# Performance work log

Hardware: AMD Instinct MI355X
Metric: run time of the kernel (lower is better)

Reference implementation:

```python
import jax, jax.numpy as jnp
import numpy as np

HID = 512
HEADS = 8
DH = HID // HEADS


def setup_inputs() -> dict:
    key = jax.random.key(0)
    ks = jax.random.split(key, 20)
    B, L = 4, 256
    s = 1.0 / np.sqrt(HID)
    sh = 1.0 / np.sqrt(DH)
    inp = {
        'query': jax.random.normal(ks[0], (B, L, HID), jnp.float32),
        'key':   jax.random.normal(ks[1], (B, L, HID), jnp.float32),
        'value': jax.random.normal(ks[2], (B, L, HID), jnp.float32),
        'Wq': jax.random.uniform(ks[3], (HID, HID), jnp.float32, -s, s),
        'bq': jax.random.uniform(ks[4], (HID,), jnp.float32, -s, s),
        'Wk': jax.random.uniform(ks[5], (HID, HID), jnp.float32, -s, s),
        'bk': jax.random.uniform(ks[6], (HID,), jnp.float32, -s, s),
        'Wv': jax.random.uniform(ks[7], (HID, HID), jnp.float32, -s, s),
        'bv': jax.random.uniform(ks[8], (HID,), jnp.float32, -s, s),
        'W1': jax.random.uniform(ks[9], (DH, DH), jnp.float32, -sh, sh),
        'b1': jax.random.uniform(ks[10], (DH,), jnp.float32, -sh, sh),
        'W2': jax.random.uniform(ks[11], (DH, DH), jnp.float32, -sh, sh),
        'b2': jax.random.uniform(ks[12], (DH,), jnp.float32, -sh, sh),
        'va_w': jax.random.uniform(ks[13], (1, DH), jnp.float32, -sh, sh),
        'va_b': jax.random.uniform(ks[14], (1,), jnp.float32, -sh, sh),
        'Wo': jax.random.uniform(ks[15], (HID, HID), jnp.float32, -s, s),
        'bo': jax.random.uniform(ks[16], (HID,), jnp.float32, -s, s),
    }
    return inp


def reference(query, key, value, Wq, bq, Wk, bk, Wv, bv, W1, b1, W2, b2, va_w, va_b, Wo, bo):
    B, Lq, _ = query.shape
    Lk = key.shape[1]
    # projections + split heads -> [B, H, L, Dh]
    Q = (query @ Wq.T + bq).reshape(B, Lq, HEADS, DH).transpose(0, 2, 1, 3)
    K = (key   @ Wk.T + bk).reshape(B, Lk, HEADS, DH).transpose(0, 2, 1, 3)
    V = (value @ Wv.T + bv).reshape(B, Lk, HEADS, DH).transpose(0, 2, 1, 3)
    Qt = Q @ W1.T + b1  # [B,H,Lq,Dh]
    Kt = K @ W2.T + b2  # [B,H,Lk,Dh]
    # additive (Bahdanau) scores: va . tanh(q_i + k_j) + b over head_dim
    pair = jnp.tanh(Qt[:, :, :, None, :] + Kt[:, :, None, :, :])  # [B,H,Lq,Lk,Dh]
    energy = jnp.einsum('bhqkd,d->bhqk', pair, va_w[0]) + va_b[0]
    attention = jax.nn.softmax(energy, axis=-1)
    x = jnp.einsum('bhqk,bhkd->bhqd', attention, V)
    x = x.transpose(0, 2, 1, 3).reshape(B, Lq, HID)
    out = x @ Wo.T + bo
    return out, attention
```

## Files before the change

### kernel.cpp

```cpp
#include <hip/hip_runtime.h>

#define HIDN 512
#define NHEAD 8
#define DHEAD 64
#define NB 4
#define NL 256
#define NROW 1024

#define SCALE2 2.8853900817779268f
#define LOG2E  1.4426950408889634f
#define NEG2LOG2E -2.8853900817779268f

#define WS_WQB 0
#define WS_WKB (WS_WQB + 131072)
#define WS_BQF (WS_WKB + 131072)
#define WS_BKF (WS_BQF + 512)
#define WS_QBF (WS_BKF + 512)
#define WS_KBF (WS_QBF + 262144)
#define WS_VBF (WS_KBF + 262144)
#define WS_WVB (WS_VBF + 262144)
#define WS_WOB (WS_WVB + 131072)
#define WS_EQ  (WS_WOB + 131072)
#define WS_EK  (WS_EQ + 524288)
#define WS_VF  (WS_EK + 524288)

typedef __attribute__((ext_vector_type(4))) float f32x4;
typedef __attribute__((ext_vector_type(8))) short bf16x8;

__device__ __forceinline__ short f2bf(float x) {
  unsigned u = __float_as_uint(x);
  u += 0x7fffu + ((u >> 16) & 1u);
  return (short)(u >> 16);
}

__global__ __launch_bounds__(256) void prep(
    const float* __restrict__ Wq, const float* __restrict__ bq,
    const float* __restrict__ Wk, const float* __restrict__ bk,
    const float* __restrict__ W1, const float* __restrict__ b1,
    const float* __restrict__ W2, const float* __restrict__ b2,
    const float* __restrict__ q, const float* __restrict__ k, const float* __restrict__ v,
    const float* __restrict__ Wv, const float* __restrict__ Wo,
    float* __restrict__ ws)
{
  const int z = blockIdx.z;
  if (z >= 2) {
    const int zz = z - 2;
    const float* src; short* dst; int n;
    if (zz == 0)      { src = q;  dst = (short*)(ws + WS_QBF); n = 524288; }
    else if (zz == 1) { src = k;  dst = (short*)(ws + WS_KBF); n = 524288; }
    else if (zz == 2) { src = v;  dst = (short*)(ws + WS_VBF); n = 524288; }
    else if (zz == 3) { src = Wv; dst = (short*)(ws + WS_WVB); n = 262144; }
    else              { src = Wo; dst = (short*)(ws + WS_WOB); n = 262144; }
    const int i = (blockIdx.x * 256 + threadIdx.x) * 8;
    if (i >= n) return;
    const float4 a = *reinterpret_cast<const float4*>(src + i);
    const float4 b = *reinterpret_cast<const float4*>(src + i + 4);
    bf16x8 o;
    o[0] = f2bf(a.x); o[1] = f2bf(a.y); o[2] = f2bf(a.z); o[3] = f2bf(a.w);
    o[4] = f2bf(b.x); o[5] = f2bf(b.y); o[6] = f2bf(b.z); o[7] = f2bf(b.w);
    *reinterpret_cast<bf16x8*>(dst + i) = o;
    return;
  }

  if (blockIdx.x >= 128) return;
  const int c0 = (blockIdx.x & 3) * 128;
  const int y  = blockIdx.x >> 2;
  const int h  = y >> 2;
  const int ig = y & 3;
  const int which = z;
  const float* Wsrc = which ? Wk : Wq;
  const float* bsrc = which ? bk : bq;
  const float* Wt   = which ? W2 : W1;
  const float* bt   = which ? b2 : b1;
  short* Wout = reinterpret_cast<short*>(ws + (which ? WS_WKB : WS_WQB));
  float* bout = ws + (which ? WS_BKF : WS_BQF);

  __shared__ float Wtl[16][68];
  for (int t = threadIdx.x; t < 16*64; t += 256)
    Wtl[t >> 6][t & 63] = Wt[(ig*16 + (t >> 6))*64 + (t & 63)];
  __syncthreads();

  const int c  = c0 + (threadIdx.x & 127);
  const int i0 = (threadIdx.x >> 7) * 8;
  float acc[8];
#pragma unroll
  for (int ii = 0; ii < 8; ++ii) acc[ii] = 0.f;

  for (int j0 = 0; j0 < 64; j0 += 4) {
    const float s0 = Wsrc[(h*64 + j0 + 0)*HIDN + c];
    const float s1 = Wsrc[(h*64 + j0 + 1)*HIDN + c];
    const float s2 = Wsrc[(h*64 + j0 + 2)*HIDN + c];
    const float s3 = Wsrc[(h*64 + j0 + 3)*HIDN + c];
#pragma unroll
    for (int ii = 0; ii < 8; ++ii) {
      const float4 wv4 = *reinterpret_cast<const float4*>(&Wtl[i0+ii][j0]);
      float a = acc[ii];
      a = fmaf(wv4.x, s0, a);
      a = fmaf(wv4.y, s1, a);
      a = fmaf(wv4.z, s2, a);
      a = fmaf(wv4.w, s3, a);
      acc[ii] = a;
    }
  }
#pragma unroll
  for (int ii = 0; ii < 8; ++ii)
    Wout[(h*64 + ig*16 + i0 + ii)*HIDN + c] = f2bf(acc[ii] * SCALE2);

  if (blockIdx.x == 0 && threadIdx.x < 16) {
    const int il = threadIdx.x;
    float a = bt[ig*16 + il];
    for (int j = 0; j < 64; ++j)
      a = fmaf(Wtl[il][j], bsrc[h*64 + j], a);
    bout[h*64 + ig*16 + il] = a * SCALE2;
  }
}

__global__ __launch_bounds__(256) void mfma_proj(float* __restrict__ ws, const float* __restrict__ bv)
{
  const int z = blockIdx.z;
  const short* A; const short* W; const float* bias;
  if (z == 0)      { A = (const short*)(ws + WS_QBF); W = (const short*)(ws + WS_WQB); bias = ws + WS_BQF; }
  else if (z == 1) { A = (const short*)(ws + WS_KBF); W = (const short*)(ws + WS_WKB); bias = ws + WS_BKF; }
  else             { A = (const short*)(ws + WS_VBF); W = (const short*)(ws + WS_WVB); bias = bv; }

  const int wid  = threadIdx.x >> 6;
  const int lane = threadIdx.x & 63;
  const int mt = blockIdx.y * 4 + wid;
  const int nb = blockIdx.x * 32;
  const short* aptr = A + (mt*16 + (lane & 15))*HIDN + (lane >> 4)*8;
  const short* wptr = W + (nb + (lane & 15))*HIDN + (lane >> 4)*8;

  f32x4 acc[2] = {{0,0,0,0},{0,0,0,0}};
#pragma unroll 4
  for (int k0 = 0; k0 < HIDN; k0 += 32) {
    const bf16x8 af = *reinterpret_cast<const bf16x8*>(aptr + k0);
    const short* wp = wptr + k0;
#pragma unroll
    for (int t = 0; t < 2; ++t)
      acc[t] = __builtin_amdgcn_mfma_f32_16x16x32_bf16(
          af, *reinterpret_cast<const bf16x8*>(wp + t*16*HIDN), acc[t], 0, 0, 0);
  }

  const int rbase = mt*16 + (lane >> 4)*4;
  if (z < 2) {
    float* dst = ws + (z == 0 ? WS_EQ : WS_EK);
#pragma unroll
    for (int t = 0; t < 2; ++t) {
      const int c = nb + t*16 + (lane & 15);
      const float bc = bias[c];
      const int hh = c >> 6, d = c & 63;
#pragma unroll
      for (int r = 0; r < 4; ++r) {
        const int R = rbase + r;
        dst[(((R >> 8)*NHEAD + hh)*NL + (R & 255))*DHEAD + d] =
            __builtin_amdgcn_exp2f(acc[t][r] + bc);
      }
    }
  } else {
    short* vf = reinterpret_cast<short*>(ws + WS_VF);
#pragma unroll
    for (int t = 0; t < 2; ++t) {
      const int c = nb + t*16 + (lane & 15);
      const float bc = bias[c];
      const int hh = c >> 6, d = c & 63;
#pragma unroll
      for (int r = 0; r < 4; ++r) {
        const int R = rbase + r;
        const int l = R & 255;
        const int bh = (R >> 8)*NHEAD + hh;
        const int tile = ((l >> 5) << 2) + (d >> 4);
        const int lanep = (((l >> 3) & 3) << 4) + (d & 15);
        vf[((bh*32 + tile)*64 + lanep)*8 + (l & 7)] = f2bf(acc[t][r] + bc);
      }
    }
  }
}

__global__ __launch_bounds__(256) void mfma_out(
    float* __restrict__ ws, const float* __restrict__ bo, float* __restrict__ out)
{
  const short* A = (const short*)(ws + WS_QBF);
  const short* W = (const short*)(ws + WS_WOB);
  const int wid  = threadIdx.x >> 6;
  const int lane = threadIdx.x & 63;
  const int mt = blockIdx.y * 4 + wid;
  const int nb = blockIdx.x * 32;
  const short* aptr = A + (mt*16 + (lane & 15))*HIDN + (lane >> 4)*8;
  const short* wptr = W + (nb + (lane & 15))*HIDN + (lane >> 4)*8;

  f32x4 acc[2] = {{0,0,0,0},{0,0,0,0}};
#pragma unroll 4
  for (int k0 = 0; k0 < HIDN; k0 += 32) {
    const bf16x8 af = *reinterpret_cast<const bf16x8*>(aptr + k0);
    const short* wp = wptr + k0;
#pragma unroll
    for (int t = 0; t < 2; ++t)
      acc[t] = __builtin_amdgcn_mfma_f32_16x16x32_bf16(
          af, *reinterpret_cast<const bf16x8*>(wp + t*16*HIDN), acc[t], 0, 0, 0);
  }

  const int rbase = mt*16 + (lane >> 4)*4;
#pragma unroll
  for (int t = 0; t < 2; ++t) {
    const int c = nb + t*16 + (lane & 15);
    const float bc = bo[c];
#pragma unroll
    for (int r = 0; r < 4; ++r)
      out[(rbase + r)*HIDN + c] = acc[t][r] + bc;
  }
}

__global__ __launch_bounds__(1024, 8) void attn_kernel(
    const float* __restrict__ eqB, const float* __restrict__ ekB,
    const short* __restrict__ vfB, const float* __restrict__ va_w,
    float* __restrict__ attn_out, short* __restrict__ xb)
{
  const int qt = blockIdx.x;
  const int bh = blockIdx.y;
  const int tid = threadIdx.x;

  __shared__ __align__(16) short aLb[8][64][8];
  __shared__ __align__(16) float reds[4][4][4];

  const float* EKB = ekB + bh*NL*DHEAD;
  const short* VF  = vfB + bh*32*64*8;

  const int g  = tid >> 8;
  const int lk = tid & 255;
  const int wv = lk >> 6;
  const int l  = lk & 63;
  const float* EkRow = EKB + lk*DHEAD;
  const int g_u = __builtin_amdgcn_readfirstlane(g);
  const float* EqG = eqB + (bh*NL + qt*16 + g_u*4)*DHEAD;

  float acc[4];
#pragma unroll
  for (int qi = 0; qi < 4; ++qi) acc[qi] = 0.f;

#pragma unroll 1
  for (int d0 = 0; d0 < 64; d0 += 8) {
    const f32x4 ea = *reinterpret_cast<const f32x4*>(EkRow + d0);
    const f32x4 eb = *reinterpret_cast<const f32x4*>(EkRow + d0 + 4);
    const f32x4 vaA = *reinterpret_cast<const f32x4*>(va_w + d0);
    const f32x4 vaB = *reinterpret_cast<const f32x4*>(va_w + d0 + 4);
#pragma unroll
    for (int qi = 0; qi < 4; ++qi) {
      const f32x4 qa = *reinterpret_cast<const f32x4*>(EqG + qi*DHEAD + d0);
      const f32x4 qb = *reinterpret_cast<const f32x4*>(EqG + qi*DHEAD + d0 + 4);
      const float t0 = fmaf(qa.x, ea.x, 1.0f);
      const float t1 = fmaf(qa.y, ea.y, 1.0f);
      const float t2 = fmaf(qa.z, ea.z, 1.0f);
      const float t3 = fmaf(qa.w, ea.w, 1.0f);
      const float t4 = fmaf(qb.x, eb.x, 1.0f);
      const float t5 = fmaf(qb.y, eb.y, 1.0f);
      const float t6 = fmaf(qb.z, eb.z, 1.0f);
      const float t7 = fmaf(qb.w, eb.w, 1.0f);
      float a = acc[qi];
      a = fmaf(fmaf(vaA.x, t1, vaA.y * t0), __builtin_amdgcn_rcpf(t0 * t1), a);
      a = fmaf(fmaf(vaA.z, t3, vaA.w * t2), __builtin_amdgcn_rcpf(t2 * t3), a);
      a = fmaf(fmaf(vaB.x, t5, vaB.y * t4), __builtin_amdgcn_rcpf(t4 * t5), a);
      a = fmaf(fmaf(vaB.z, t7, vaB.w * t6), __builtin_amdgcn_rcpf(t6 * t7), a);
      acc[qi] = a;
    }
  }

  float p[4];
#pragma unroll
  for (int qi = 0; qi < 4; ++qi)
    p[qi] = __builtin_amdgcn_exp2f(acc[qi] * NEG2LOG2E);

#pragma unroll
  for (int qi = 0; qi < 4; ++qi) {
    float s = p[qi];
#pragma unroll
    for (int off = 1; off < 64; off <<= 1)
      s += __shfl_xor(s, off);
    if (l == 0) reds[g][wv][qi] = s;
  }
  {
    const int kb2 = lk >> 5;
    const int lbase = ((lk >> 3) & 3) * 16;
    const int jb = lk & 7;
#pragma unroll
    for (int qi = 0; qi < 4; ++qi)
      aLb[kb2][lbase + g*4 + qi][jb] = f2bf(p[qi]);
  }
  __syncthreads();

  {
    f32x4 s4 = {0.f,0.f,0.f,0.f};
#pragma unroll
    for (int w2 = 0; w2 < 4; ++w2)
      s4 += *reinterpret_cast<const f32x4*>(&reds[g][w2][0]);
    float inv[4];
    inv[0] = __builtin_amdgcn_rcpf(s4.x); inv[1] = __builtin_amdgcn_rcpf(s4.y);
    inv[2] = __builtin_amdgcn_rcpf(s4.z); inv[3] = __builtin_amdgcn_rcpf(s4.w);
#pragma unroll
    for (int qi = 0; qi < 4; ++qi)
      attn_out[(bh*NL + qt*16 + g*4 + qi)*NL + lk] = p[qi] * inv[qi];

    const int wid = tid >> 6;
    if (wid < 4) {
      f32x4 pacc = {0.f,0.f,0.f,0.f};
#pragma unroll
      for (int kb2 = 0; kb2 < 8; ++kb2) {
        const bf16x8 af  = *reinterpret_cast<const bf16x8*>(&aLb[kb2][l][0]);
        const bf16x8 bff = *reinterpret_cast<const bf16x8*>(&VF[((kb2*4 + wid)*64 + l)*8]);
        pacc = __builtin_amdgcn_mfma_f32_16x16x32_bf16(af, bff, pacc, 0, 0, 0);
      }
      const int b_ = bh >> 3, hh = bh & 7;
      const int colv = hh*DHEAD + wid*16 + (l & 15);
#pragma unroll
      for (int r = 0; r < 4; ++r) {
        const int row = (l >> 4)*4 + r;
        const float stot = reds[row>>2][0][row&3] + reds[row>>2][1][row&3]
                         + reds[row>>2][2][row&3] + reds[row>>2][3][row&3];
        xb[(b_*NL + qt*16 + row)*HIDN + colv] = f2bf(pacc[r] * __builtin_amdgcn_rcpf(stot));
      }
    }
  }
}

extern "C" void kernel_launch(void* const* d_in, const int* in_sizes, int n_in,
                              void* d_out, int out_size, void* d_ws, size_t ws_size,
                              hipStream_t stream) {
  const float* query = (const float*)d_in[0];
  const float* key   = (const float*)d_in[1];
  const float* value = (const float*)d_in[2];
  const float* Wq = (const float*)d_in[3];
  const float* bq = (const float*)d_in[4];
  const float* Wk = (const float*)d_in[5];
  const float* bk = (const float*)d_in[6];
  const float* Wv = (const float*)d_in[7];
  const float* bv = (const float*)d_in[8];
  const float* W1 = (const float*)d_in[9];
  const float* b1 = (const float*)d_in[10];
  const float* W2 = (const float*)d_in[11];
  const float* b2 = (const float*)d_in[12];
  const float* va_w = (const float*)d_in[13];
  const float* Wo = (const float*)d_in[15];
  const float* bo = (const float*)d_in[16];

  float* out = (float*)d_out;
  float* ws  = (float*)d_ws;
  float* attn = out + NROW*HIDN;

  prep<<<dim3(256, 1, 7), 256, 0, stream>>>(Wq, bq, Wk, bk, W1, b1, W2, b2,
                                            query, key, value, Wv, Wo, ws);
  mfma_proj<<<dim3(16, 16, 3), 256, 0, stream>>>(ws, bv);
  attn_kernel<<<dim3(16, 32), 1024, 0, stream>>>(
      ws + WS_EQ, ws + WS_EK, (const short*)(ws + WS_VF), va_w,
      attn, (short*)(ws + WS_QBF));
  mfma_out<<<dim3(16, 16), 256, 0, stream>>>(ws, bo, out);
}
```

Measured before the change: 59.64 us.

## Fuse all four stages into one cooperative persistent kernel with grid syncs

Replaces the four separate launches (prep, projection GEMMs, attention, output GEMM) with a single cooperative kernel of 256 blocks of 1024 threads. Stages are separated by grid-wide barriers, and each block emulates several of the old 256-thread blocks or runs two attention tiles in sequence. The aim is to remove kernel launch gaps and per-launch overhead. In exchange it pays for grid.sync barriers, runs the smaller stages at fixed 1024-thread granularity with idle sub-blocks, and halves parallelism in the attention stage.

After: 197.7 us. 3.31x slower.

```diff
diff --git a/kernel.cpp b/kernel.cpp
--- a/kernel.cpp
+++ b/kernel.cpp
@@ -1,4 +1,7 @@
 #include <hip/hip_runtime.h>
+#include <hip/hip_cooperative_groups.h>
+
+namespace cg = cooperative_groups;
 
 #define HIDN 512
 #define NHEAD 8
@@ -33,289 +36,307 @@
   return (short)(u >> 16);
 }
 
-__global__ __launch_bounds__(256) void prep(
+__global__ __launch_bounds__(1024, 4) void fused_all(
+    const float* __restrict__ q, const float* __restrict__ kin, const float* __restrict__ v,
     const float* __restrict__ Wq, const float* __restrict__ bq,
     const float* __restrict__ Wk, const float* __restrict__ bk,
+    const float* __restrict__ Wv, const float* __restrict__ bv,
     const float* __restrict__ W1, const float* __restrict__ b1,
     const float* __restrict__ W2, const float* __restrict__ b2,
-    const float* __restrict__ q, const float* __restrict__ k, const float* __restrict__ v,
-    const float* __restrict__ Wv, const float* __restrict__ Wo,
-    float* __restrict__ ws)
+    const float* __restrict__ va_w, const float* __restrict__ Wo,
+    const float* __restrict__ bo,
+    float* __restrict__ ws, float* __restrict__ out)
 {
-  const int z = blockIdx.z;
-  if (z >= 2) {
-    const int zz = z - 2;
-    const float* src; short* dst; int n;
-    if (zz == 0)      { src = q;  dst = (short*)(ws + WS_QBF); n = 524288; }
-    else if (zz == 1) { src = k;  dst = (short*)(ws + WS_KBF); n = 524288; }
-    else if (zz == 2) { src = v;  dst = (short*)(ws + WS_VBF); n = 524288; }
-    else if (zz == 3) { src = Wv; dst = (short*)(ws + WS_WVB); n = 262144; }
-    else              { src = Wo; dst = (short*)(ws + WS_WOB); n = 262144; }
-    const int i = (blockIdx.x * 256 + threadIdx.x) * 8;
-    if (i >= n) return;
-    const float4 a = *reinterpret_cast<const float4*>(src + i);
-    const float4 b = *reinterpret_cast<const float4*>(src + i + 4);
+  cg::grid_group grid = cg::this_grid();
+  const int bid = blockIdx.x;
+  const int tid = threadIdx.x;
+  const int sub = tid >> 8;
+  const int lt  = tid & 255;
+
+  __shared__ __align__(16) float WtlS[4][16][68];
+  __shared__ __align__(16) short aLb[8][64][8];
+  __shared__ __align__(16) float reds[4][4][4];
+
+  float* attn_out = out + NROW*HIDN;
+
+  {
+    const int ci = bid * 1024 + tid;
+    const int i = ci * 8;
+    const float* src; short* dst; int rel;
+    if (i < 524288)        { src = q;   dst = (short*)(ws + WS_QBF); rel = i; }
+    else if (i < 1048576)  { src = kin; dst = (short*)(ws + WS_KBF); rel = i - 524288; }
+    else if (i < 1572864)  { src = v;   dst = (short*)(ws + WS_VBF); rel = i - 1048576; }
+    else if (i < 1835008)  { src = Wv;  dst = (short*)(ws + WS_WVB); rel = i - 1572864; }
+    else                   { src = Wo;  dst = (short*)(ws + WS_WOB); rel = i - 1835008; }
+    const float4 a = *reinterpret_cast<const float4*>(src + rel);
+    const float4 b = *reinterpret_cast<const float4*>(src + rel + 4);
     bf16x8 o;
     o[0] = f2bf(a.x); o[1] = f2bf(a.y); o[2] = f2bf(a.z); o[3] = f2bf(a.w);
     o[4] = f2bf(b.x); o[5] = f2bf(b.y); o[6] = f2bf(b.z); o[7] = f2bf(b.w);
-    *reinterpret_cast<bf16x8*>(dst + i) = o;
-    return;
-  }
-
-  if (blockIdx.x >= 128) return;
-  const int c0 = (blockIdx.x & 3) * 128;
-  const int y  = blockIdx.x >> 2;
-  const int h  = y >> 2;
-  const int ig = y & 3;
-  const int which = z;
-  const float* Wsrc = which ? Wk : Wq;
-  const float* bsrc = which ? bk : bq;
-  const float* Wt   = which ? W2 : W1;
-  const float* bt   = which ? b2 : b1;
-  short* Wout = reinterpret_cast<short*>(ws + (which ? WS_WKB : WS_WQB));
-  float* bout = ws + (which ? WS_BKF : WS_BQF);
-
-  __shared__ float Wtl[16][68];
-  for (int t = threadIdx.x; t < 16*64; t += 256)
-    Wtl[t >> 6][t & 63] = Wt[(ig*16 + (t >> 6))*64 + (t & 63)];
-  __syncthreads();
-
-  const int c  = c0 + (threadIdx.x & 127);
-  const int i0 = (threadIdx.x >> 7) * 8;
-  float acc[8];
-#pragma unroll
-  for (int ii = 0; ii < 8; ++ii) acc[ii] = 0.f;
-
-  for (int j0 = 0; j0 < 64; j0 += 4) {
-    const float s0 = Wsrc[(h*64 + j0 + 0)*HIDN + c];
-    const float s1 = Wsrc[(h*64 + j0 + 1)*HIDN + c];
-    const float s2 = Wsrc[(h*64 + j0 + 2)*HIDN + c];
-    const float s3 = Wsrc[(h*64 + j0 + 3)*HIDN + c];
-#pragma unroll
-    for (int ii = 0; ii < 8; ++ii) {
-      const float4 wv4 = *reinterpret_cast<const float4*>(&Wtl[i0+ii][j0]);
-      float a = acc[ii];
-      a = fmaf(wv4.x, s0, a);
-      a = fmaf(wv4.y, s1, a);
-      a = fmaf(wv4.z, s2, a);
-      a = fmaf(wv4.w, s3, a);
-      acc[ii] = a;
-    }
-  }
-#pragma unroll
-  for (int ii = 0; ii < 8; ++ii)
-    Wout[(h*64 + ig*16 + i0 + ii)*HIDN + c] = f2bf(acc[ii] * SCALE2);
-
-  if (blockIdx.x == 0 && threadIdx.x < 16) {
-    const int il = threadIdx.x;
-    float a = bt[ig*16 + il];
-    for (int j = 0; j < 64; ++j)
-      a = fmaf(Wtl[il][j], bsrc[h*64 + j], a);
-    bout[h*64 + ig*16 + il] = a * SCALE2;
-  }
-}
-
-__global__ __launch_bounds__(256) void mfma_proj(float* __restrict__ ws, const float* __restrict__ bv)
-{
-  const int z = blockIdx.z;
-  const short* A; const short* W; const float* bias;
-  if (z == 0)      { A = (const short*)(ws + WS_QBF); W = (const short*)(ws + WS_WQB); bias = ws + WS_BQF; }
-  else if (z == 1) { A = (const short*)(ws + WS_KBF); W = (const short*)(ws + WS_WKB); bias = ws + WS_BKF; }
-  else             { A = (const short*)(ws + WS_VBF); W = (const short*)(ws + WS_WVB); bias = bv; }
-
-  const int wid  = threadIdx.x >> 6;
-  const int lane = threadIdx.x & 63;
-  const int mt = blockIdx.y * 4 + wid;
-  const int nb = blockIdx.x * 32;
-  const short* aptr = A + (mt*16 + (lane & 15))*HIDN + (lane >> 4)*8;
-  const short* wptr = W + (nb + (lane & 15))*HIDN + (lane >> 4)*8;
-
-  f32x4 acc[2] = {{0,0,0,0},{0,0,0,0}};
+    *reinterpret_cast<bf16x8*>(dst + rel) = o;
+  }
+  if (bid < 64) {
+    const int vb = bid*4 + sub;
+    const int which = vb >> 7;
+    const int y  = (vb >> 2) & 31;
+    const int h  = y >> 2;
+    const int ig = y & 3;
+    const int c0 = (vb & 3) * 128;
+    const float* Wsrc = which ? Wk : Wq;
+    const float* bsrc = which ? bk : bq;
+    const float* Wt   = which ? W2 : W1;
+    const float* bt   = which ? b2 : b1;
+    short* Wout = (short*)(ws + (which ? WS_WKB : WS_WQB));
+    float* bout = ws + (which ? WS_BKF : WS_BQF);
+    float (*Wtl)[68] = WtlS[sub];
+
+    for (int t = lt; t < 16*64; t += 256)
+      Wtl[t >> 6][t & 63] = Wt[(ig*16 + (t >> 6))*64 + (t & 63)];
+    __syncthreads();
+
+    const int c  = c0 + (lt & 127);
+    const int i0 = (lt >> 7) * 8;
+    float acc[8];
+#pragma unroll
+    for (int ii = 0; ii < 8; ++ii) acc[ii] = 0.f;
+    for (int j0 = 0; j0 < 64; j0 += 4) {
+      const float s0 = Wsrc[(h*64 + j0 + 0)*HIDN + c];
+      const float s1 = Wsrc[(h*64 + j0 + 1)*HIDN + c];
+      const float s2 = Wsrc[(h*64 + j0 + 2)*HIDN + c];
+      const float s3 = Wsrc[(h*64 + j0 + 3)*HIDN + c];
+#pragma unroll
+      for (int ii = 0; ii < 8; ++ii) {
+        const float4 wv4 = *reinterpret_cast<const float4*>(&Wtl[i0+ii][j0]);
+        float a = acc[ii];
+        a = fmaf(wv4.x, s0, a);
+        a = fmaf(wv4.y, s1, a);
+        a = fmaf(wv4.z, s2, a);
+        a = fmaf(wv4.w, s3, a);
+        acc[ii] = a;
+      }
+    }
+#pragma unroll
+    for (int ii = 0; ii < 8; ++ii)
+      Wout[(h*64 + ig*16 + i0 + ii)*HIDN + c] = f2bf(acc[ii] * SCALE2);
+
+    if ((vb & 3) == 0 && lt < 16) {
+      const int il = lt;
+      float a = bt[ig*16 + il];
+      for (int j = 0; j < 64; ++j)
+        a = fmaf(Wtl[il][j], bsrc[h*64 + j], a);
+      bout[h*64 + ig*16 + il] = a * SCALE2;
+    }
+  }
+  grid.sync();
+
+  {
+    const int vb = bid*4 + sub;
+    if (vb < 768) {
+      const int z  = vb >> 8;
+      const int r  = vb & 255;
+      const int bx = r & 15;
+      const int by = r >> 4;
+      const short* A; const short* W; const float* bias;
+      if (z == 0)      { A = (const short*)(ws + WS_QBF); W = (const short*)(ws + WS_WQB); bias = ws + WS_BQF; }
+      else if (z == 1) { A = (const short*)(ws + WS_KBF); W = (const short*)(ws + WS_WKB); bias = ws + WS_BKF; }
+      else             { A = (const short*)(ws + WS_VBF); W = (const short*)(ws + WS_WVB); bias = bv; }
+
+      const int wid  = lt >> 6;
+      const int lane = lt & 63;
+      const int mt = by*4 + wid;
+      const int nb = bx*32;
+      const short* aptr = A + (mt*16 + (lane & 15))*HIDN + (lane >> 4)*8;
+      const short* wptr = W + (nb + (lane & 15))*HIDN + (lane >> 4)*8;
+
+      f32x4 acc[2] = {{0,0,0,0},{0,0,0,0}};
 #pragma unroll 4
-  for (int k0 = 0; k0 < HIDN; k0 += 32) {
-    const bf16x8 af = *reinterpret_cast<const bf16x8*>(aptr + k0);
-    const short* wp = wptr + k0;
-#pragma unroll
-    for (int t = 0; t < 2; ++t)
-      acc[t] = __builtin_amdgcn_mfma_f32_16x16x32_bf16(
-          af, *reinterpret_cast<const bf16x8*>(wp + t*16*HIDN), acc[t], 0, 0, 0);
-  }
-
-  const int rbase = mt*16 + (lane >> 4)*4;
-  if (z < 2) {
-    float* dst = ws + (z == 0 ? WS_EQ : WS_EK);
-#pragma unroll
-    for (int t = 0; t < 2; ++t) {
-      const int c = nb + t*16 + (lane & 15);
-      const float bc = bias[c];
-      const int hh = c >> 6, d = c & 63;
-#pragma unroll
-      for (int r = 0; r < 4; ++r) {
-        const int R = rbase + r;
-        dst[(((R >> 8)*NHEAD + hh)*NL + (R & 255))*DHEAD + d] =
-            __builtin_amdgcn_exp2f(acc[t][r] + bc);
-      }
-    }
-  } else {
-    short* vf = reinterpret_cast<short*>(ws + WS_VF);
-#pragma unroll
-    for (int t = 0; t < 2; ++t) {
-      const int c = nb + t*16 + (lane & 15);
-      const float bc = bias[c];
-      const int hh = c >> 6, d = c & 63;
-#pragma unroll
-      for (int r = 0; r < 4; ++r) {
-        const int R = rbase + r;
-        const int l = R & 255;
-        const int bh = (R >> 8)*NHEAD + hh;
-        const int tile = ((l >> 5) << 2) + (d >> 4);
-        const int lanep = (((l >> 3) & 3) << 4) + (d & 15);
-        vf[((bh*32 + tile)*64 + lanep)*8 + (l & 7)] = f2bf(acc[t][r] + bc);
-      }
-    }
-  }
-}
-
-__global__ __launch_bounds__(256) void mfma_out(
-    float* __restrict__ ws, const float* __restrict__ bo, float* __restrict__ out)
-{
-  const short* A = (const short*)(ws + WS_QBF);
-  const short* W = (const short*)(ws + WS_WOB);
-  const int wid  = threadIdx.x >> 6;
-  const int lane = threadIdx.x & 63;
-  const int mt = blockIdx.y * 4 + wid;
-  const int nb = blockIdx.x * 32;
-  const short* aptr = A + (mt*16 + (lane & 15))*HIDN + (lane >> 4)*8;
-  const short* wptr = W + (nb + (lane & 15))*HIDN + (lane >> 4)*8;
-
-  f32x4 acc[2] = {{0,0,0,0},{0,0,0,0}};
+      for (int k0 = 0; k0 < HIDN; k0 += 32) {
+        const bf16x8 af = *reinterpret_cast<const bf16x8*>(aptr + k0);
+        const short* wp = wptr + k0;
+#pragma unroll
+        for (int t = 0; t < 2; ++t)
+          acc[t] = __builtin_amdgcn_mfma_f32_16x16x32_bf16(
+              af, *reinterpret_cast<const bf16x8*>(wp + t*16*HIDN), acc[t], 0, 0, 0);
+      }
+
+      const int rbase = mt*16 + (lane >> 4)*4;
+      if (z < 2) {
+        float* dst = ws + (z == 0 ? WS_EQ : WS_EK);
+#pragma unroll
+        for (int t = 0; t < 2; ++t) {
+          const int c = nb + t*16 + (lane & 15);
+          const float bc = bias[c];
+          const int hh = c >> 6, d = c & 63;
+#pragma unroll
+          for (int r2 = 0; r2 < 4; ++r2) {
+            const int R = rbase + r2;
+            dst[(((R >> 8)*NHEAD + hh)*NL + (R & 255))*DHEAD + d] =
+                __builtin_amdgcn_exp2f(acc[t][r2] + bc);
+          }
+        }
+      } else {
+        short* vf = (short*)(ws + WS_VF);
+#pragma unroll
+        for (int t = 0; t < 2; ++t) {
+          const int c = nb + t*16 + (lane & 15);
+          const float bc = bias[c];
+          const int hh = c >> 6, d = c & 63;
+#pragma unroll
+          for (int r2 = 0; r2 < 4; ++r2) {
+            const int R = rbase + r2;
+            const int l = R & 255;
+            const int bh = (R >> 8)*NHEAD + hh;
+            const int tile = ((l >> 5) << 2) + (d >> 4);
+            const int lanep = (((l >> 3) & 3) << 4) + (d & 15);
+            vf[((bh*32 + tile)*64 + lanep)*8 + (l & 7)] = f2bf(acc[t][r2] + bc);
+          }
+        }
+      }
+    }
+  }
+  grid.sync();
+
+  {
+    short* xb = (short*)(ws + WS_QBF);
+    for (int pass = 0; pass < 2; ++pass) {
+      const int vb = bid + pass*256;
+      const int qt = vb & 15;
+      const int bh = vb >> 4;
+      const float* EKB = ws + WS_EK + bh*NL*DHEAD;
+      const short* VF  = (const short*)(ws + WS_VF) + bh*32*64*8;
+
+      const int g  = tid >> 8;
+      const int lk = tid & 255;
+      const int wv = lk >> 6;
+      const int l  = lk & 63;
+      const float* EkRow = EKB + lk*DHEAD;
+      const int g_u = __builtin_amdgcn_readfirstlane(g);
+      const float* EqG = ws + WS_EQ + (bh*NL + qt*16 + g_u*4)*DHEAD;
+
+      float acc[4];
+#pragma unroll
+      for (int qi = 0; qi < 4; ++qi) acc[qi] = 0.f;
+
+#pragma unroll 1
+      for (int d0 = 0; d0 < 64; d0 += 8) {
+        const f32x4 ea = *reinterpret_cast<const f32x4*>(EkRow + d0);
+        const f32x4 eb = *reinterpret_cast<const f32x4*>(EkRow + d0 + 4);
+        const f32x4 vaA = *reinterpret_cast<const f32x4*>(va_w + d0);
+        const f32x4 vaB = *reinterpret_cast<const f32x4*>(va_w + d0 + 4);
+#pragma unroll
+        for (int qi = 0; qi < 4; ++qi) {
+          const f32x4 qa = *reinterpret_cast<const f32x4*>(EqG + qi*DHEAD + d0);
+          const f32x4 qb = *reinterpret_cast<const f32x4*>(EqG + qi*DHEAD + d0 + 4);
+          const float t0 = fmaf(qa.x, ea.x, 1.0f);
+          const float t1 = fmaf(qa.y, ea.y, 1.0f);
+          const float t2 = fmaf(qa.z, ea.z, 1.0f);
+          const float t3 = fmaf(qa.w, ea.w, 1.0f);
+          const float t4 = fmaf(qb.x, eb.x, 1.0f);
+          const float t5 = fmaf(qb.y, eb.y, 1.0f);
+          const float t6 = fmaf(qb.z, eb.z, 1.0f);
+          const float t7 = fmaf(qb.w, eb.w, 1.0f);
+          float a = acc[qi];
+          a = fmaf(fmaf(vaA.x, t1, vaA.y * t0), __builtin_amdgcn_rcpf(t0 * t1), a);
+          a = fmaf(fmaf(vaA.z, t3, vaA.w * t2), __builtin_amdgcn_rcpf(t2 * t3), a);
+          a = fmaf(fmaf(vaB.x, t5, vaB.y * t4), __builtin_amdgcn_rcpf(t4 * t5), a);
+          a = fmaf(fmaf(vaB.z, t7, vaB.w * t6), __builtin_amdgcn_rcpf(t6 * t7), a);
+          acc[qi] = a;
+        }
+      }
+
+      float p[4];
+#pragma unroll
+      for (int qi = 0; qi < 4; ++qi)
+        p[qi] = __builtin_amdgcn_exp2f(acc[qi] * NEG2LOG2E);
+
+#pragma unroll
+      for (int qi = 0; qi < 4; ++qi) {
+        float s = p[qi];
+#pragma unroll
+        for (int off = 1; off < 64; off <<= 1)
+          s += __shfl_xor(s, off);
+        if (l == 0) reds[g][wv][qi] = s;
+      }
+      {
+        const int kb2 = lk >> 5;
+        const int lbase = ((lk >> 3) & 3) * 16;
+        const int jb = lk & 7;
+#pragma unroll
+        for (int qi = 0; qi < 4; ++qi)
+          aLb[kb2][lbase + g*4 + qi][jb] = f2bf(p[qi]);
+      }
+      __syncthreads();
+
+      {
+        f32x4 s4 = {0.f,0.f,0.f,0.f};
+#pragma unroll
+        for (int w2 = 0; w2 < 4; ++w2)
+          s4 += *reinterpret_cast<const f32x4*>(&reds[g][w2][0]);
+        float inv[4];
+        inv[0] = __builtin_amdgcn_rcpf(s4.x); inv[1] = __builtin_amdgcn_rcpf(s4.y);
+        inv[2] = __builtin_amdgcn_rcpf(s4.z); inv[3] = __builtin_amdgcn_rcpf(s4.w);
+#pragma unroll
+        for (int qi = 0; qi < 4; ++qi)
+          attn_out[(bh*NL + qt*16 + g*4 + qi)*NL + lk] = p[qi] * inv[qi];
+
+        const int wid = tid >> 6;
+        if (wid < 4) {
+          f32x4 pacc = {0.f,0.f,0.f,0.f};
+#pragma unroll
+          for (int kb2 = 0; kb2 < 8; ++kb2) {
+            const bf16x8 af  = *reinterpret_cast<const bf16x8*>(&aLb[kb2][l][0]);
+            const bf16x8 bff = *reinterpret_cast<const bf16x8*>(&VF[((kb2*4 + wid)*64 + l)*8]);
+            pacc = __builtin_amdgcn_mfma_f32_16x16x32_bf16(af, bff, pacc, 0, 0, 0);
+          }
+          const int b_ = bh >> 3, hh = bh & 7;
+          const int colv = hh*DHEAD + wid*16 + (l & 15);
+#pragma unroll
+          for (int r2 = 0; r2 < 4; ++r2) {
+            const int row = (l >> 4)*4 + r2;
+            const float stot = reds[row>>2][0][row&3] + reds[row>>2][1][row&3]
+                             + reds[row>>2][2][row&3] + reds[row>>2][3][row&3];
+            xb[(b_*NL + qt*16 + row)*HIDN + colv] = f2bf(pacc[r2] * __builtin_amdgcn_rcpf(stot));
+          }
+        }
+      }
+      __syncthreads();
+    }
+  }
+  grid.sync();
+
+  {
+    const int vb = bid*4 + sub;
+    if (vb < 256) {
+      const int bx = vb & 15;
+      const int by = vb >> 4;
+      const short* A = (const short*)(ws + WS_QBF);
+      const short* W = (const short*)(ws + WS_WOB);
+      const int wid  = lt >> 6;
+      const int lane = lt & 63;
+      const int mt = by*4 + wid;
+      const int nb = bx*32;
+      const short* aptr = A + (mt*16 + (lane & 15))*HIDN + (lane >> 4)*8;
+      const short* wptr = W + (nb + (lane & 15))*HIDN + (lane >> 4)*8;
+
+      f32x4 acc[2] = {{0,0,0,0},{0,0,0,0}};
 #pragma unroll 4
-  for (int k0 = 0; k0 < HIDN; k0 += 32) {
-    const bf16x8 af = *reinterpret_cast<const bf16x8*>(aptr + k0);
-    const short* wp = wptr + k0;
-#pragma unroll
-    for (int t = 0; t < 2; ++t)
-      acc[t] = __builtin_amdgcn_mfma_f32_16x16x32_bf16(
-          af, *reinterpret_cast<const bf16x8*>(wp + t*16*HIDN), acc[t], 0, 0, 0);
-  }
-
-  const int rbase = mt*16 + (lane >> 4)*4;
-#pragma unroll
-  for (int t = 0; t < 2; ++t) {
-    const int c = nb + t*16 + (lane & 15);
-    const float bc = bo[c];
-#pragma unroll
-    for (int r = 0; r < 4; ++r)
-      out[(rbase + r)*HIDN + c] = acc[t][r] + bc;
-  }
-}
-
-__global__ __launch_bounds__(1024, 8) void attn_kernel(
-    const float* __restrict__ eqB, const float* __restrict__ ekB,
-    const short* __restrict__ vfB, const float* __restrict__ va_w,
-    float* __restrict__ attn_out, short* __restrict__ xb)
-{
-  const int qt = blockIdx.x;
-  const int bh = blockIdx.y;
-  const int tid = threadIdx.x;
-
-  __shared__ __align__(16) short aLb[8][64][8];
-  __shared__ __align__(16) float reds[4][4][4];
-
-  const float* EKB = ekB + bh*NL*DHEAD;
-  const short* VF  = vfB + bh*32*64*8;
-
-  const int g  = tid >> 8;
-  const int lk = tid & 255;
-  const int wv = lk >> 6;
-  const int l  = lk & 63;
-  const float* EkRow = EKB + lk*DHEAD;
-  const int g_u = __builtin_amdgcn_readfirstlane(g);
-  const float* EqG = eqB + (bh*NL + qt*16 + g_u*4)*DHEAD;
-
-  float acc[4];
-#pragma unroll
-  for (int qi = 0; qi < 4; ++qi) acc[qi] = 0.f;
-
-#pragma unroll 1
-  for (int d0 = 0; d0 < 64; d0 += 8) {
-    const f32x4 ea = *reinterpret_cast<const f32x4*>(EkRow + d0);
-    const f32x4 eb = *reinterpret_cast<const f32x4*>(EkRow + d0 + 4);
-    const f32x4 vaA = *reinterpret_cast<const f32x4*>(va_w + d0);
-    const f32x4 vaB = *reinterpret_cast<const f32x4*>(va_w + d0 + 4);
-#pragma unroll
-    for (int qi = 0; qi < 4; ++qi) {
-      const f32x4 qa = *reinterpret_cast<const f32x4*>(EqG + qi*DHEAD + d0);
-      const f32x4 qb = *reinterpret_cast<const f32x4*>(EqG + qi*DHEAD + d0 + 4);
-      const float t0 = fmaf(qa.x, ea.x, 1.0f);
-      const float t1 = fmaf(qa.y, ea.y, 1.0f);
-      const float t2 = fmaf(qa.z, ea.z, 1.0f);
-      const float t3 = fmaf(qa.w, ea.w, 1.0f);
-      const float t4 = fmaf(qb.x, eb.x, 1.0f);
-      const float t5 = fmaf(qb.y, eb.y, 1.0f);
-      const float t6 = fmaf(qb.z, eb.z, 1.0f);
-      const float t7 = fmaf(qb.w, eb.w, 1.0f);
-      float a = acc[qi];
-      a = fmaf(fmaf(vaA.x, t1, vaA.y * t0), __builtin_amdgcn_rcpf(t0 * t1), a);
-      a = fmaf(fmaf(vaA.z, t3, vaA.w * t2), __builtin_amdgcn_rcpf(t2 * t3), a);
-      a = fmaf(fmaf(vaB.x, t5, vaB.y * t4), __builtin_amdgcn_rcpf(t4 * t5), a);
-      a = fmaf(fmaf(vaB.z, t7, vaB.w * t6), __builtin_amdgcn_rcpf(t6 * t7), a);
-      acc[qi] = a;
-    }
-  }
-
-  float p[4];
-#pragma unroll
-  for (int qi = 0; qi < 4; ++qi)
-    p[qi] = __builtin_amdgcn_exp2f(acc[qi] * NEG2LOG2E);
-
-#pragma unroll
-  for (int qi = 0; qi < 4; ++qi) {
-    float s = p[qi];
-#pragma unroll
-    for (int off = 1; off < 64; off <<= 1)
-      s += __shfl_xor(s, off);
-    if (l == 0) reds[g][wv][qi] = s;
-  }
-  {
-    const int kb2 = lk >> 5;
-    const int lbase = ((lk >> 3) & 3) * 16;
-    const int jb = lk & 7;
-#pragma unroll
-    for (int qi = 0; qi < 4; ++qi)
-      aLb[kb2][lbase + g*4 + qi][jb] = f2bf(p[qi]);
-  }
-  __syncthreads();
-
-  {
-    f32x4 s4 = {0.f,0.f,0.f,0.f};
-#pragma unroll
-    for (int w2 = 0; w2 < 4; ++w2)
-      s4 += *reinterpret_cast<const f32x4*>(&reds[g][w2][0]);
-    float inv[4];
-    inv[0] = __builtin_amdgcn_rcpf(s4.x); inv[1] = __builtin_amdgcn_rcpf(s4.y);
-    inv[2] = __builtin_amdgcn_rcpf(s4.z); inv[3] = __builtin_amdgcn_rcpf(s4.w);
-#pragma unroll
-    for (int qi = 0; qi < 4; ++qi)
-      attn_out[(bh*NL + qt*16 + g*4 + qi)*NL + lk] = p[qi] * inv[qi];
-
-    const int wid = tid >> 6;
-    if (wid < 4) {
-      f32x4 pacc = {0.f,0.f,0.f,0.f};
-#pragma unroll
-      for (int kb2 = 0; kb2 < 8; ++kb2) {
-        const bf16x8 af  = *reinterpret_cast<const bf16x8*>(&aLb[kb2][l][0]);
-        const bf16x8 bff = *reinterpret_cast<const bf16x8*>(&VF[((kb2*4 + wid)*64 + l)*8]);
-        pacc = __builtin_amdgcn_mfma_f32_16x16x32_bf16(af, bff, pacc, 0, 0, 0);
-      }
-      const int b_ = bh >> 3, hh = bh & 7;
-      const int colv = hh*DHEAD + wid*16 + (l & 15);
-#pragma unroll
-      for (int r = 0; r < 4; ++r) {
-        const int row = (l >> 4)*4 + r;
-        const float stot = reds[row>>2][0][row&3] + reds[row>>2][1][row&3]
-                         + reds[row>>2][2][row&3] + reds[row>>2][3][row&3];
-        xb[(b_*NL + qt*16 + row)*HIDN + colv] = f2bf(pacc[r] * __builtin_amdgcn_rcpf(stot));
+      for (int k0 = 0; k0 < HIDN; k0 += 32) {
+        const bf16x8 af = *reinterpret_cast<const bf16x8*>(aptr + k0);
+        const short* wp = wptr + k0;
+#pragma unroll
+        for (int t = 0; t < 2; ++t)
+          acc[t] = __builtin_amdgcn_mfma_f32_16x16x32_bf16(
+              af, *reinterpret_cast<const bf16x8*>(wp + t*16*HIDN), acc[t], 0, 0, 0);
+      }
+
+      const int rbase = mt*16 + (lane >> 4)*4;
+#pragma unroll
+      for (int t = 0; t < 2; ++t) {
+        const int c = nb + t*16 + (lane & 15);
+        const float bc = bo[c];
+#pragma unroll
+        for (int r2 = 0; r2 < 4; ++r2)
+          out[(rbase + r2)*HIDN + c] = acc[t][r2] + bc;
       }
     }
   }
@@ -324,32 +345,33 @@
 extern "C" void kernel_launch(void* const* d_in, const int* in_sizes, int n_in,
                               void* d_out, int out_size, void* d_ws, size_t ws_size,
                               hipStream_t stream) {
-  const float* query = (const float*)d_in[0];
-  const float* key   = (const float*)d_in[1];
-  const float* value = (const float*)d_in[2];
-  const float* Wq = (const float*)d_in[3];
-  const float* bq = (const float*)d_in[4];
-  const float* Wk = (const float*)d_in[5];
-  const float* bk = (const float*)d_in[6];
-  const float* Wv = (const float*)d_in[7];
-  const float* bv = (const float*)d_in[8];
-  const float* W1 = (const float*)d_in[9];
-  const float* b1 = (const float*)d_in[10];
-  const float* W2 = (const float*)d_in[11];
-  const float* b2 = (const float*)d_in[12];
+  const float* q    = (const float*)d_in[0];
+  const float* kin  = (const float*)d_in[1];
+  const float* v    = (const float*)d_in[2];
+  const float* Wq   = (const float*)d_in[3];
+  const float* bq   = (const float*)d_in[4];
+  const float* Wk   = (const float*)d_in[5];
+  const float* bk   = (const float*)d_in[6];
+  const float* Wv   = (const float*)d_in[7];
+  const float* bv   = (const float*)d_in[8];
+  const float* W1   = (const float*)d_in[9];
+  const float* b1   = (const float*)d_in[10];
+  const float* W2   = (const float*)d_in[11];
+  const float* b2   = (const float*)d_in[12];
   const float* va_w = (const float*)d_in[13];
-  const float* Wo = (const float*)d_in[15];
-  const float* bo = (const float*)d_in[16];
+  const float* Wo   = (const float*)d_in[15];
+  const float* bo   = (const float*)d_in[16];
 
   float* out = (float*)d_out;
   float* ws  = (float*)d_ws;
-  float* attn = out + NROW*HIDN;
-
-  prep<<<dim3(256, 1, 7), 256, 0, stream>>>(Wq, bq, Wk, bk, W1, b1, W2, b2,
-                                            query, key, value, Wv, Wo, ws);
-  mfma_proj<<<dim3(16, 16, 3), 256, 0, stream>>>(ws, bv);
-  attn_kernel<<<dim3(16, 32), 1024, 0, stream>>>(
-      ws + WS_EQ, ws + WS_EK, (const short*)(ws + WS_VF), va_w,
-      attn, (short*)(ws + WS_QBF));
-  mfma_out<<<dim3(16, 16), 256, 0, stream>>>(ws, bo, out);
+
+  void* args[] = {
+    (void*)&q, (void*)&kin, (void*)&v,
+    (void*)&Wq, (void*)&bq, (void*)&Wk, (void*)&bk, (void*)&Wv, (void*)&bv,
+    (void*)&W1, (void*)&b1, (void*)&W2, (void*)&b2,
+    (void*)&va_w, (void*)&Wo, (void*)&bo,
+    (void*)&ws, (void*)&out
+  };
+  hipLaunchCooperativeKernel((const void*)fused_all, dim3(256), dim3(1024),
+                             args, 0, stream);
 }
```

## Fuse bf16 conversion and per-head transform into projection kernel, drop prep pass

Applied to the files above, without the earlier changes.

Removes the separate prep kernel that converted inputs and weights to bf16 and prefolded W1/W2 into Wq/Wk. The new proj2 kernel converts fp32 operands to bf16 on the fly, computes the 16x64 per-head projection, stages it in shared memory and applies the 64x64 head transform with a second MFMA before the exp2 epilogue. The output projection also converts Wo on the fly. This saves one launch and the conversion traffic through the workspace. In exchange each block rereads fp32 data with twice the bytes, and the extra bf16 rounding of the intermediate projection changes precision slightly.

Result: slower. 83.23 us (+39.6%).

```diff
diff --git a/kernel.cpp b/kernel.cpp
--- a/kernel.cpp
+++ b/kernel.cpp
@@ -8,21 +8,12 @@
 #define NROW 1024
 
 #define SCALE2 2.8853900817779268f
-#define LOG2E  1.4426950408889634f
 #define NEG2LOG2E -2.8853900817779268f
 
-#define WS_WQB 0
-#define WS_WKB (WS_WQB + 131072)
-#define WS_BQF (WS_WKB + 131072)
-#define WS_BKF (WS_BQF + 512)
-#define WS_QBF (WS_BKF + 512)
-#define WS_KBF (WS_QBF + 262144)
-#define WS_VBF (WS_KBF + 262144)
-#define WS_WVB (WS_VBF + 262144)
-#define WS_WOB (WS_WVB + 131072)
-#define WS_EQ  (WS_WOB + 131072)
+#define WS_EQ  0
 #define WS_EK  (WS_EQ + 524288)
 #define WS_VF  (WS_EK + 524288)
+#define WS_X   (WS_VF + 262144)
 
 typedef __attribute__((ext_vector_type(4))) float f32x4;
 typedef __attribute__((ext_vector_type(8))) short bf16x8;
@@ -33,180 +24,87 @@
   return (short)(u >> 16);
 }
 
-__global__ __launch_bounds__(256) void prep(
+__device__ __forceinline__ bf16x8 cvt8(const float* __restrict__ p) {
+  const float4 a = *reinterpret_cast<const float4*>(p);
+  const float4 b = *reinterpret_cast<const float4*>(p + 4);
+  bf16x8 o;
+  o[0] = f2bf(a.x); o[1] = f2bf(a.y); o[2] = f2bf(a.z); o[3] = f2bf(a.w);
+  o[4] = f2bf(b.x); o[5] = f2bf(b.y); o[6] = f2bf(b.z); o[7] = f2bf(b.w);
+  return o;
+}
+
+__global__ __launch_bounds__(256) void proj2(
+    const float* __restrict__ q, const float* __restrict__ kin, const float* __restrict__ v,
     const float* __restrict__ Wq, const float* __restrict__ bq,
     const float* __restrict__ Wk, const float* __restrict__ bk,
+    const float* __restrict__ Wv, const float* __restrict__ bv,
     const float* __restrict__ W1, const float* __restrict__ b1,
     const float* __restrict__ W2, const float* __restrict__ b2,
-    const float* __restrict__ q, const float* __restrict__ k, const float* __restrict__ v,
-    const float* __restrict__ Wv, const float* __restrict__ Wo,
     float* __restrict__ ws)
 {
-  const int z = blockIdx.z;
-  if (z >= 2) {
-    const int zz = z - 2;
-    const float* src; short* dst; int n;
-    if (zz == 0)      { src = q;  dst = (short*)(ws + WS_QBF); n = 524288; }
-    else if (zz == 1) { src = k;  dst = (short*)(ws + WS_KBF); n = 524288; }
-    else if (zz == 2) { src = v;  dst = (short*)(ws + WS_VBF); n = 524288; }
-    else if (zz == 3) { src = Wv; dst = (short*)(ws + WS_WVB); n = 262144; }
-    else              { src = Wo; dst = (short*)(ws + WS_WOB); n = 262144; }
-    const int i = (blockIdx.x * 256 + threadIdx.x) * 8;
-    if (i >= n) return;
-    const float4 a = *reinterpret_cast<const float4*>(src + i);
-    const float4 b = *reinterpret_cast<const float4*>(src + i + 4);
-    bf16x8 o;
-    o[0] = f2bf(a.x); o[1] = f2bf(a.y); o[2] = f2bf(a.z); o[3] = f2bf(a.w);
-    o[4] = f2bf(b.x); o[5] = f2bf(b.y); o[6] = f2bf(b.z); o[7] = f2bf(b.w);
-    *reinterpret_cast<bf16x8*>(dst + i) = o;
-    return;
-  }
-
-  if (blockIdx.x >= 128) return;
-  const int c0 = (blockIdx.x & 3) * 128;
-  const int y  = blockIdx.x >> 2;
-  const int h  = y >> 2;
-  const int ig = y & 3;
-  const int which = z;
-  const float* Wsrc = which ? Wk : Wq;
-  const float* bsrc = which ? bk : bq;
-  const float* Wt   = which ? W2 : W1;
-  const float* bt   = which ? b2 : b1;
-  short* Wout = reinterpret_cast<short*>(ws + (which ? WS_WKB : WS_WQB));
-  float* bout = ws + (which ? WS_BKF : WS_BQF);
-
-  __shared__ float Wtl[16][68];
-  for (int t = threadIdx.x; t < 16*64; t += 256)
-    Wtl[t >> 6][t & 63] = Wt[(ig*16 + (t >> 6))*64 + (t & 63)];
-  __syncthreads();
-
-  const int c  = c0 + (threadIdx.x & 127);
-  const int i0 = (threadIdx.x >> 7) * 8;
-  float acc[8];
-#pragma unroll
-  for (int ii = 0; ii < 8; ++ii) acc[ii] = 0.f;
-
-  for (int j0 = 0; j0 < 64; j0 += 4) {
-    const float s0 = Wsrc[(h*64 + j0 + 0)*HIDN + c];
-    const float s1 = Wsrc[(h*64 + j0 + 1)*HIDN + c];
-    const float s2 = Wsrc[(h*64 + j0 + 2)*HIDN + c];
-    const float s3 = Wsrc[(h*64 + j0 + 3)*HIDN + c];
-#pragma unroll
-    for (int ii = 0; ii < 8; ++ii) {
-      const float4 wv4 = *reinterpret_cast<const float4*>(&Wtl[i0+ii][j0]);
-      float a = acc[ii];
-      a = fmaf(wv4.x, s0, a);
-      a = fmaf(wv4.y, s1, a);
-      a = fmaf(wv4.z, s2, a);
-      a = fmaf(wv4.w, s3, a);
-      acc[ii] = a;
-    }
-  }
-#pragma unroll
-  for (int ii = 0; ii < 8; ++ii)
-    Wout[(h*64 + ig*16 + i0 + ii)*HIDN + c] = f2bf(acc[ii] * SCALE2);
-
-  if (blockIdx.x == 0 && threadIdx.x < 16) {
-    const int il = threadIdx.x;
-    float a = bt[ig*16 + il];
-    for (int j = 0; j < 64; ++j)
-      a = fmaf(Wtl[il][j], bsrc[h*64 + j], a);
-    bout[h*64 + ig*16 + il] = a * SCALE2;
-  }
-}
-
-__global__ __launch_bounds__(256) void mfma_proj(float* __restrict__ ws, const float* __restrict__ bv)
-{
-  const int z = blockIdx.z;
-  const short* A; const short* W; const float* bias;
-  if (z == 0)      { A = (const short*)(ws + WS_QBF); W = (const short*)(ws + WS_WQB); bias = ws + WS_BQF; }
-  else if (z == 1) { A = (const short*)(ws + WS_KBF); W = (const short*)(ws + WS_WKB); bias = ws + WS_BKF; }
-  else             { A = (const short*)(ws + WS_VBF); W = (const short*)(ws + WS_WVB); bias = bv; }
-
-  const int wid  = threadIdx.x >> 6;
-  const int lane = threadIdx.x & 63;
-  const int mt = blockIdx.y * 4 + wid;
-  const int nb = blockIdx.x * 32;
-  const short* aptr = A + (mt*16 + (lane & 15))*HIDN + (lane >> 4)*8;
-  const short* wptr = W + (nb + (lane & 15))*HIDN + (lane >> 4)*8;
-
-  f32x4 acc[2] = {{0,0,0,0},{0,0,0,0}};
+  const int mt = blockIdx.x;
+  const int h  = blockIdx.y;
+  const int z  = blockIdx.z;
+  const int w  = threadIdx.x >> 6;
+  const int l  = threadIdx.x & 63;
+
+  const float* A  = (z == 0) ? q  : (z == 1) ? kin : v;
+  const float* Ws = (z == 0) ? Wq : (z == 1) ? Wk  : Wv;
+  const float* bs = (z == 0) ? bq : (z == 1) ? bk  : bv;
+
+  __shared__ __align__(16) short Pl[16][72];
+
+  const int colh = w*16 + (l & 15);
+  const float* aptr = A  + (mt*16 + (l & 15))*HIDN + (l >> 4)*8;
+  const float* wptr = Ws + (h*64 + colh)*HIDN + (l >> 4)*8;
+
+  f32x4 acc = {0.f, 0.f, 0.f, 0.f};
 #pragma unroll 4
   for (int k0 = 0; k0 < HIDN; k0 += 32) {
-    const bf16x8 af = *reinterpret_cast<const bf16x8*>(aptr + k0);
-    const short* wp = wptr + k0;
-#pragma unroll
-    for (int t = 0; t < 2; ++t)
-      acc[t] = __builtin_amdgcn_mfma_f32_16x16x32_bf16(
-          af, *reinterpret_cast<const bf16x8*>(wp + t*16*HIDN), acc[t], 0, 0, 0);
-  }
-
-  const int rbase = mt*16 + (lane >> 4)*4;
-  if (z < 2) {
+    const bf16x8 af = cvt8(aptr + k0);
+    const bf16x8 bf = cvt8(wptr + k0);
+    acc = __builtin_amdgcn_mfma_f32_16x16x32_bf16(af, bf, acc, 0, 0, 0);
+  }
+  const float bc = bs[h*64 + colh];
+
+  if (z == 2) {
+    short* vf = reinterpret_cast<short*>(ws + WS_VF);
+#pragma unroll
+    for (int r = 0; r < 4; ++r) {
+      const int R = mt*16 + (l >> 4)*4 + r;
+      const int l2 = R & 255;
+      const int bh = (R >> 8)*NHEAD + h;
+      const int tile = ((l2 >> 5) << 2) + (colh >> 4);
+      const int lanep = (((l2 >> 3) & 3) << 4) + (colh & 15);
+      vf[((bh*32 + tile)*64 + lanep)*8 + (l2 & 7)] = f2bf(acc[r] + bc);
+    }
+  } else {
+#pragma unroll
+    for (int r = 0; r < 4; ++r)
+      Pl[(l >> 4)*4 + r][colh] = f2bf(acc[r] + bc);
+    __syncthreads();
+
+    const float* Wt = (z == 0) ? W1 : W2;
+    const float* bt = (z == 0) ? b1 : b2;
+    const short* pp  = &Pl[l & 15][(l >> 4)*8];
+    const float* wtp = Wt + colh*64 + (l >> 4)*8;
+
+    f32x4 acc2 = {0.f, 0.f, 0.f, 0.f};
+#pragma unroll
+    for (int j0 = 0; j0 < 64; j0 += 32) {
+      const bf16x8 af = *reinterpret_cast<const bf16x8*>(pp + j0);
+      const bf16x8 bf = cvt8(wtp + j0);
+      acc2 = __builtin_amdgcn_mfma_f32_16x16x32_bf16(af, bf, acc2, 0, 0, 0);
+    }
+    const float btc = bt[colh];
     float* dst = ws + (z == 0 ? WS_EQ : WS_EK);
 #pragma unroll
-    for (int t = 0; t < 2; ++t) {
-      const int c = nb + t*16 + (lane & 15);
-      const float bc = bias[c];
-      const int hh = c >> 6, d = c & 63;
-#pragma unroll
-      for (int r = 0; r < 4; ++r) {
-        const int R = rbase + r;
-        dst[(((R >> 8)*NHEAD + hh)*NL + (R & 255))*DHEAD + d] =
-            __builtin_amdgcn_exp2f(acc[t][r] + bc);
-      }
-    }
-  } else {
-    short* vf = reinterpret_cast<short*>(ws + WS_VF);
-#pragma unroll
-    for (int t = 0; t < 2; ++t) {
-      const int c = nb + t*16 + (lane & 15);
-      const float bc = bias[c];
-      const int hh = c >> 6, d = c & 63;
-#pragma unroll
-      for (int r = 0; r < 4; ++r) {
-        const int R = rbase + r;
-        const int l = R & 255;
-        const int bh = (R >> 8)*NHEAD + hh;
-        const int tile = ((l >> 5) << 2) + (d >> 4);
-        const int lanep = (((l >> 3) & 3) << 4) + (d & 15);
-        vf[((bh*32 + tile)*64 + lanep)*8 + (l & 7)] = f2bf(acc[t][r] + bc);
-      }
-    }
-  }
-}
-
-__global__ __launch_bounds__(256) void mfma_out(
-    float* __restrict__ ws, const float* __restrict__ bo, float* __restrict__ out)
-{
-  const short* A = (const short*)(ws + WS_QBF);
-  const short* W = (const short*)(ws + WS_WOB);
-  const int wid  = threadIdx.x >> 6;
-  const int lane = threadIdx.x & 63;
-  const int mt = blockIdx.y * 4 + wid;
-  const int nb = blockIdx.x * 32;
-  const short* aptr = A + (mt*16 + (lane & 15))*HIDN + (lane >> 4)*8;
-  const short* wptr = W + (nb + (lane & 15))*HIDN + (lane >> 4)*8;
-
-  f32x4 acc[2] = {{0,0,0,0},{0,0,0,0}};
-#pragma unroll 4
-  for (int k0 = 0; k0 < HIDN; k0 += 32) {
-    const bf16x8 af = *reinterpret_cast<const bf16x8*>(aptr + k0);
-    const short* wp = wptr + k0;
-#pragma unroll
-    for (int t = 0; t < 2; ++t)
-      acc[t] = __builtin_amdgcn_mfma_f32_16x16x32_bf16(
-          af, *reinterpret_cast<const bf16x8*>(wp + t*16*HIDN), acc[t], 0, 0, 0);
-  }
-
-  const int rbase = mt*16 + (lane >> 4)*4;
-#pragma unroll
-  for (int t = 0; t < 2; ++t) {
-    const int c = nb + t*16 + (lane & 15);
-    const float bc = bo[c];
-#pragma unroll
-    for (int r = 0; r < 4; ++r)
-      out[(rbase + r)*HIDN + c] = acc[t][r] + bc;
+    for (int r = 0; r < 4; ++r) {
+      const int R = mt*16 + (l >> 4)*4 + r;
+      const int bh = (R >> 8)*NHEAD + h;
+      dst[(bh*NL + (R & 255))*DHEAD + colh] =
+          __builtin_amdgcn_exp2f(SCALE2 * (acc2[r] + btc));
+    }
   }
 }
 
@@ -321,35 +219,68 @@
   }
 }
 
+__global__ __launch_bounds__(256) void mfma_out(
+    const short* __restrict__ Xb, const float* __restrict__ Wo,
+    const float* __restrict__ bo, float* __restrict__ out)
+{
+  const int wid  = threadIdx.x >> 6;
+  const int lane = threadIdx.x & 63;
+  const int mt = blockIdx.y * 4 + wid;
+  const int nb = blockIdx.x * 32;
+  const short* aptr = Xb + (mt*16 + (lane & 15))*HIDN + (lane >> 4)*8;
+  const float* wptr = Wo + (nb + (lane & 15))*HIDN + (lane >> 4)*8;
+
+  f32x4 acc[2] = {{0,0,0,0},{0,0,0,0}};
+#pragma unroll 4
+  for (int k0 = 0; k0 < HIDN; k0 += 32) {
+    const bf16x8 af = *reinterpret_cast<const bf16x8*>(aptr + k0);
+#pragma unroll
+    for (int t = 0; t < 2; ++t) {
+      const bf16x8 bf = cvt8(wptr + t*16*HIDN + k0);
+      acc[t] = __builtin_amdgcn_mfma_f32_16x16x32_bf16(af, bf, acc[t], 0, 0, 0);
+    }
+  }
+
+  const int rbase = mt*16 + (lane >> 4)*4;
+#pragma unroll
+  for (int t = 0; t < 2; ++t) {
+    const int c = nb + t*16 + (lane & 15);
+    const float bc = bo[c];
+#pragma unroll
+    for (int r = 0; r < 4; ++r)
+      out[(rbase + r)*HIDN + c] = acc[t][r] + bc;
+  }
+}
+
 extern "C" void kernel_launch(void* const* d_in, const int* in_sizes, int n_in,
                               void* d_out, int out_size, void* d_ws, size_t ws_size,
                               hipStream_t stream) {
-  const float* query = (const float*)d_in[0];
-  const float* key   = (const float*)d_in[1];
-  const float* value = (const float*)d_in[2];
-  const float* Wq = (const float*)d_in[3];
-  const float* bq = (const float*)d_in[4];
-  const float* Wk = (const float*)d_in[5];
-  const float* bk = (const float*)d_in[6];
-  const float* Wv = (const float*)d_in[7];
-  const float* bv = (const float*)d_in[8];
-  const float* W1 = (const float*)d_in[9];
-  const float* b1 = (const float*)d_in[10];
-  const float* W2 = (const float*)d_in[11];
-  const float* b2 = (const float*)d_in[12];
+  const float* q    = (const float*)d_in[0];
+  const float* kin  = (const float*)d_in[1];
+  const float* v    = (const float*)d_in[2];
+  const float* Wq   = (const float*)d_in[3];
+  const float* bq   = (const float*)d_in[4];
+  const float* Wk   = (const float*)d_in[5];
+  const float* bk   = (const float*)d_in[6];
+  const float* Wv   = (const float*)d_in[7];
+  const float* bv   = (const float*)d_in[8];
+  const float* W1   = (const float*)d_in[9];
+  const float* b1   = (const float*)d_in[10];
+  const float* W2   = (const float*)d_in[11];
+  const float* b2   = (const float*)d_in[12];
   const float* va_w = (const float*)d_in[13];
-  const float* Wo = (const float*)d_in[15];
-  const float* bo = (const float*)d_in[16];
+  const float* Wo   = (const float*)d_in[15];
+  const float* bo   = (const float*)d_in[16];
 
   float* out = (float*)d_out;
   float* ws  = (float*)d_ws;
   float* attn = out + NROW*HIDN;
 
-  prep<<<dim3(256, 1, 7), 256, 0, stream>>>(Wq, bq, Wk, bk, W1, b1, W2, b2,
-                                            query, key, value, Wv, Wo, ws);
-  mfma_proj<<<dim3(16, 16, 3), 256, 0, stream>>>(ws, bv);
+  proj2<<<dim3(64, 8, 3), 256, 0, stream>>>(q, kin, v, Wq, bq, Wk, bk, Wv, bv,
+                                            W1, b1, W2, b2, ws);
   attn_kernel<<<dim3(16, 32), 1024, 0, stream>>>(
       ws + WS_EQ, ws + WS_EK, (const short*)(ws + WS_VF), va_w,
-      attn, (short*)(ws + WS_QBF));
-  mfma_out<<<dim3(16, 16), 256, 0, stream>>>(ws, bo, out);
-}
+      attn, (short*)(ws + WS_X));
+  mfma_out<<<dim3(16, 16), 256, 0, stream>>>(
+      (const short*)(ws + WS_X), Wo, bo, out);
+}
```
